# Performance work log

Measured on AMD Instinct MI355X. Metric: run time of the kernel, lower is better.

## Reference

```python
import jax, jax.numpy as jnp
import numpy as np

# 3D multi-scale deformable attention (MSDeformAttn, n_heads=8 / 3D variant)
LEVEL_SHAPES = [(32, 32, 32), (16, 16, 16), (8, 8, 8), (4, 4, 4)]  # (H, W, D) per level
D_MODEL, N_HEADS, N_LEVELS, N_POINTS = 256, 8, 4, 4
C_HEAD = D_MODEL // N_HEADS  # 32
N_BATCH, LEN_Q = 1, 37440
LEN_IN = sum(h * w * d for h, w, d in LEVEL_SHAPES)  # 37440


def setup_inputs() -> dict:
    key = jax.random.key(0)
    ks = jax.random.split(key, 10)
    s = 0.02  # param init scale
    return {
        "query": jax.random.normal(ks[0], (N_BATCH, LEN_Q, D_MODEL), jnp.float32),
        "reference_points": jax.random.uniform(ks[1], (N_BATCH, LEN_Q, N_LEVELS, 3), jnp.float32),
        "input_flatten": jax.random.normal(ks[2], (N_BATCH, LEN_IN, D_MODEL), jnp.float32),
        "input_spatial_shapes": jnp.array(LEVEL_SHAPES, dtype=jnp.int32),
        "input_level_start_index": jnp.array(
            np.cumsum([0] + [h * w * d for h, w, d in LEVEL_SHAPES])[:-1], dtype=jnp.int32),
        "W_value": s * jax.random.normal(ks[3], (D_MODEL, D_MODEL), jnp.float32),
        "b_value": jnp.zeros((D_MODEL,), jnp.float32),
        "W_off": s * jax.random.normal(ks[4], (D_MODEL, N_HEADS * N_LEVELS * N_POINTS * 3), jnp.float32),
        "b_off": s * jax.random.normal(ks[5], (N_HEADS * N_LEVELS * N_POINTS * 3,), jnp.float32),
        "W_attn": s * jax.random.normal(ks[6], (D_MODEL, N_HEADS * N_LEVELS * N_POINTS), jnp.float32),
        "b_attn": jnp.zeros((N_HEADS * N_LEVELS * N_POINTS,), jnp.float32),
        "W_out": s * jax.random.normal(ks[7], (D_MODEL, D_MODEL), jnp.float32),
        "b_out": jnp.zeros((D_MODEL,), jnp.float32),
    }


def trilinear_sample(vol, gx, gy, gz):
    """torch F.grid_sample 3D, mode=bilinear, padding=zeros, align_corners=False.
    vol: (B, C, Dz, Dy, Dx); gx indexes Dx, gy indexes Dy, gz indexes Dz, each (B, Q) in [-1,1].
    Returns (B, C, Q)."""
    B, C, Dz, Dy, Dx = vol.shape
    ix = ((gx + 1.0) * Dx - 1.0) * 0.5
    iy = ((gy + 1.0) * Dy - 1.0) * 0.5
    iz = ((gz + 1.0) * Dz - 1.0) * 0.5
    x0f, y0f, z0f = jnp.floor(ix), jnp.floor(iy), jnp.floor(iz)
    fx, fy, fz = ix - x0f, iy - y0f, iz - z0f
    x0, y0, z0 = x0f.astype(jnp.int32), y0f.astype(jnp.int32), z0f.astype(jnp.int32)
    vol_f = vol.reshape(B, C, Dz * Dy * Dx)
    out = jnp.zeros((B, C, gx.shape[1]), vol.dtype)
    for dz in (0, 1):
        for dy in (0, 1):
            for dx in (0, 1):
                xc, yc, zc = x0 + dx, y0 + dy, z0 + dz
                w = ((fx if dx else 1.0 - fx) * (fy if dy else 1.0 - fy) * (fz if dz else 1.0 - fz))
                valid = ((xc >= 0) & (xc < Dx) & (yc >= 0) & (yc < Dy) & (zc >= 0) & (zc < Dz))
                idx = (jnp.clip(zc, 0, Dz - 1) * Dy + jnp.clip(yc, 0, Dy - 1)) * Dx + jnp.clip(xc, 0, Dx - 1)
                v = jnp.take_along_axis(vol_f, idx[:, None, :], axis=2)  # (B, C, Q)
                out = out + (w * valid.astype(w.dtype))[:, None, :] * v
    return out


def reference(query, reference_points, input_flatten, input_spatial_shapes,
              input_level_start_index, W_value, b_value, W_off, b_off,
              W_attn, b_attn, W_out, b_out):
    N, Lq, _ = query.shape
    Lin = input_flatten.shape[1]
    value = (input_flatten @ W_value + b_value).reshape(N, Lin, N_HEADS, C_HEAD)
    off = (query @ W_off + b_off).reshape(N, Lq, N_HEADS, N_LEVELS, N_POINTS, 3)
    attn = jax.nn.softmax((query @ W_attn + b_attn).reshape(N, Lq, N_HEADS, N_LEVELS * N_POINTS), axis=-1)
    # offset_normalizer = [W, H, D] per level (as in the torch code)
    norm = jnp.stack([input_spatial_shapes[:, 1], input_spatial_shapes[:, 0],
                      input_spatial_shapes[:, 2]], -1).astype(query.dtype)
    loc = reference_points[:, :, None, :, None, :] + off / norm[None, None, None, :, None, :]
    grids = 2.0 * loc - 1.0  # (N, Lq, M, L, P, 3)
    starts = np.cumsum([0] + [h * w * d for h, w, d in LEVEL_SHAPES])
    sampled = []
    for l, (H, W, D) in enumerate(LEVEL_SHAPES):
        vl = value[:, starts[l]:starts[l + 1]]  # (N, H*W*D, M, C)
        vol = (vl.reshape(N, H, W, D, N_HEADS, C_HEAD)
                 .transpose(0, 4, 5, 1, 2, 3)
                 .reshape(N * N_HEADS, C_HEAD, H, W, D))
        g = grids[:, :, :, l].transpose(0, 2, 1, 3, 4).reshape(N * N_HEADS, Lq * N_POINTS, 3)
        # grid x indexes last vol dim (D), y indexes W, z indexes H (torch grid_sample convention)
        s = trilinear_sample(vol, g[..., 0], g[..., 1], g[..., 2])  # (N*M, C, Lq*P)
        sampled.append(s.reshape(N * N_HEADS, C_HEAD, Lq, N_POINTS))
    samp = jnp.stack(sampled, axis=-2).reshape(N * N_HEADS, C_HEAD, Lq, N_LEVELS * N_POINTS)
    aw = attn.transpose(0, 2, 1, 3).reshape(N * N_HEADS, 1, Lq, N_LEVELS * N_POINTS)
    out = (samp * aw).sum(-1).reshape(N, N_HEADS * C_HEAD, Lq).transpose(0, 2, 1)
    return out @ W_out + b_out
```

## Files before the change

### kernel.cpp

```cpp
#include <hip/hip_runtime.h>
#include <math.h>

#define LQ      37440
#define LIN     37440
#define DMODEL  256
#define NHEADS  8
#define CHEAD   32
#define K_DIM   256

#define VALB_DELTA (LIN * 256 + 32)

typedef __attribute__((ext_vector_type(8))) short short8;
typedef __attribute__((ext_vector_type(4))) short short4v;
typedef __attribute__((ext_vector_type(4))) float f32x4;
typedef __attribute__((ext_vector_type(2))) float f32x2;

__device__ inline unsigned short bf16_rte(float f) {
    union { float f; unsigned u; } v; v.f = f;
    return (unsigned short)((v.u + 0x7fffu + ((v.u >> 16) & 1u)) >> 16);
}
__device__ inline float bf16_f(unsigned short s) {
    union { unsigned u; float f; } v; v.u = ((unsigned)s) << 16;
    return v.f;
}
__device__ inline float bits_f(unsigned u) {
    union { unsigned u; float f; } v; v.u = u;
    return v.f;
}
__device__ inline unsigned pkbf(float a, float b) {
    return (unsigned)bf16_rte(a) | ((unsigned)bf16_rte(b) << 16);
}

__device__ __forceinline__ void gl_lds16(const unsigned short* g, unsigned short* l) {
    __builtin_amdgcn_global_load_lds(
        (const __attribute__((address_space(1))) void*)g,
        (__attribute__((address_space(3))) void*)l, 16, 0, 0);
}

__global__ __launch_bounds__(256) void prep_all(
        const float* __restrict__ inp, const float* __restrict__ query,
        const float* __restrict__ Wv, const float* __restrict__ Wo,
        const float* __restrict__ Wa, const float* __restrict__ Wout,
        const float* __restrict__ bo, const float* __restrict__ ba,
        unsigned short* __restrict__ in_b, unsigned short* __restrict__ q_b,
        unsigned short* __restrict__ Bv, unsigned short* __restrict__ Bq,
        unsigned short* __restrict__ Bw, float* __restrict__ bias_m,
        unsigned short* __restrict__ padA,
        unsigned short* __restrict__ valB,
        int n4)
{
    const int bid = blockIdx.x;
    if (bid < 9360) {
        int i = bid * 256 + threadIdx.x;
        int j = i * 2;
        const float* src;
        unsigned short* dst;
        int jj;
        if (j < n4) { src = inp;   dst = in_b; jj = j; }
        else        { src = query; dst = q_b;  jj = j - n4; }
        float4 v0 = ((const float4*)src)[jj];
        float4 v1 = ((const float4*)src)[jj + 1];
        int4 o;
        o.x = (int)pkbf(v0.x, v0.y);
        o.y = (int)pkbf(v0.z, v0.w);
        o.z = (int)pkbf(v1.x, v1.y);
        o.w = (int)pkbf(v1.z, v1.w);
        ((int4*)dst)[jj >> 1] = o;
    } else {
        int i = (bid - 9360) * 256 + threadIdx.x;
        int n = i >> 8, k = i & 255;
        if (n < 256) {
            Bv[(size_t)n * 256 + k] = bf16_rte(Wv[(size_t)k * 256 + n]);
        } else if (n < 640) {
            int m = n - 256;
            Bq[(size_t)m * 256 + k] = bf16_rte(Wo[(size_t)k * 384 + m]);
        } else if (n < 768) {
            int m = n - 640;
            Bq[(size_t)(384 + m) * 256 + k] = bf16_rte(Wa[(size_t)k * 128 + m]);
        } else {
            int m = n - 768;
            Bw[(size_t)m * 256 + k] = bf16_rte(Wout[(size_t)k * 256 + m]);
        }
        if (i < 512) bias_m[i] = (i < 384) ? bo[i] : ba[i - 384];
        if (i < 64)       padA[i] = 0;
        else if (i < 96)  valB[i - 64] = 0;
        else if (i < 192) valB[(size_t)LIN * 256 + 32 + (i - 96)] = 0;
    }
}

__global__ __launch_bounds__(256) void gemm2(
    const unsigned short* __restrict__ in_b, const unsigned short* __restrict__ q_b,
    const unsigned short* __restrict__ Bv,   const unsigned short* __restrict__ Bq,
    const float* __restrict__ bv, const float* __restrict__ bias_m,
    unsigned short* __restrict__ value_t, unsigned short* __restrict__ valB,
    unsigned short* __restrict__ qbuf)
{
    __shared__ __align__(16) unsigned short SH[16384];
    unsigned short* AsL = SH;
    unsigned short* BsL = SH + 8192;

    const int t    = threadIdx.x;
    const int bm   = blockIdx.y * 128;
    const int w    = t >> 6;
    const int lane = t & 63;
    const int lm   = lane & 15;
    const int quad = lane >> 4;

    const int isval = (blockIdx.x < 2);
    const unsigned short* A  = isval ? in_b : q_b;
    const unsigned short* Bt = isval ? Bv : Bq;
    const float* bias        = isval ? bv : bias_m;
    const int n0             = (isval ? blockIdx.x : (blockIdx.x - 2)) * 128;

    const unsigned short* ga[2]; const unsigned short* gb[2];
    int loff[2];
    #pragma unroll
    for (int i = 0; i < 2; ++i) {
        int idx = i * 256 + t;
        int row = idx >> 2;
        int chn = (idx & 3) ^ ((row >> 1) & 3);
        int rga = bm + row; if (rga >= LQ) rga = LQ - 1;
        ga[i] = A  + (size_t)rga * K_DIM + chn * 8;
        gb[i] = Bt + (size_t)(n0 + row) * K_DIM + chn * 8;
        loff[i] = i * 2048 + w * 512;
    }

    const int ra0 = w * 32 + lm, ra1 = ra0 + 16;
    const int aoff0 = ra0 * 32 + ((quad ^ ((ra0 >> 1) & 3)) << 3);
    const int aoff1 = ra1 * 32 + ((quad ^ ((ra1 >> 1) & 3)) << 3);
    int boff[8];
    #pragma unroll
    for (int nt = 0; nt < 8; ++nt) {
        int rb = nt * 16 + lm;
        boff[nt] = rb * 32 + ((quad ^ ((rb >> 1) & 3)) << 3);
    }

    f32x4 acc[2][8];
    #pragma unroll
    for (int mt = 0; mt < 2; ++mt)
        #pragma unroll
        for (int nt = 0; nt < 8; ++nt)
            acc[mt][nt] = (f32x4){0.f, 0.f, 0.f, 0.f};

    #define STAGE(K0, SEL) do { \
        gl_lds16(ga[0] + (K0), AsL + (SEL) * 4096 + loff[0]); \
        gl_lds16(ga[1] + (K0), AsL + (SEL) * 4096 + loff[1]); \
        gl_lds16(gb[0] + (K0), BsL + (SEL) * 4096 + loff[0]); \
        gl_lds16(gb[1] + (K0), BsL + (SEL) * 4096 + loff[1]); \
    } while (0)

    STAGE(0, 0);
    #pragma unroll
    for (int kt = 0; kt < 8; ++kt) {
        const int sel = kt & 1;
        if (kt < 7) {
            STAGE((kt + 1) * 32, sel ^ 1);
            asm volatile("s_waitcnt vmcnt(4)" ::: "memory");
        } else {
            asm volatile("s_waitcnt vmcnt(0)" ::: "memory");
        }
        __builtin_amdgcn_s_barrier();

        const int so = sel * 4096;
        short8 af[2], bf[8];
        af[0] = *(const short8*)&AsL[so + aoff0];
        af[1] = *(const short8*)&AsL[so + aoff1];
        #pragma unroll
        for (int nt = 0; nt < 8; ++nt)
            bf[nt] = *(const short8*)&BsL[so + boff[nt]];
        #pragma unroll
        for (int mt = 0; mt < 2; ++mt)
            #pragma unroll
            for (int nt = 0; nt < 8; ++nt)
                acc[mt][nt] = __builtin_amdgcn_mfma_f32_16x16x32_bf16(af[mt], bf[nt], acc[mt][nt], 0, 0, 0);

        asm volatile("s_waitcnt lgkmcnt(0)" ::: "memory");
        __builtin_amdgcn_s_barrier();
    }
    #undef STAGE

    unsigned short* SHc = SH;
    #pragma unroll
    for (int nt = 0; nt < 8; ++nt) {
        int col = nt * 16 + lm;
        float bb = bias[n0 + col];
        #pragma unroll
        for (int mt = 0; mt < 2; ++mt) {
            int rb = w * 32 + mt * 16 + quad * 4;
            #pragma unroll
            for (int r = 0; r < 4; ++r)
                SHc[(rb + r) * 128 + col] = bf16_rte(acc[mt][nt][r] + bb);
        }
    }
    __syncthreads();

    if (isval) {
        const int h0 = n0 >> 5;
        #pragma unroll
        for (int k = 0; k < 8; ++k) {
            int ci  = t + k * 256;
            int hl  = ci >> 9;
            int rem = ci & 511;
            int row = rem >> 2;
            int cq  = (rem & 3) << 3;
            int4 v = *(const int4*)&SHc[row * 128 + hl * 32 + cq];
            int grow = bm + row;
            if (grow < LQ) {
                size_t e = ((size_t)(h0 + hl) * LIN + grow) * 32 + cq;
                *(int4*)&value_t[e] = v;
                *(int4*)&valB[32 + e] = v;
            }
        }
    } else {
        #pragma unroll
        for (int k = 0; k < 8; ++k) {
            int ci  = t + k * 256;
            int row = ci >> 4;
            int cq  = (ci & 15) << 3;
            int4 v = *(const int4*)&SHc[row * 128 + cq];
            int grow = bm + row;
            if (grow < LQ)
                *(int4*)&qbuf[(size_t)grow * 512 + n0 + cq] = v;
        }
    }
}

__global__ __launch_bounds__(256) void gemm_out(
    const unsigned short* __restrict__ A, const unsigned short* __restrict__ Bt,
    const float* __restrict__ bias, float* __restrict__ Cout)
{
    __shared__ __align__(16) unsigned short SH[16384];
    unsigned short* AsL = SH;
    unsigned short* BsL = SH + 8192;

    const int t    = threadIdx.x;
    const int bm   = blockIdx.y * 128;
    const int n0   = blockIdx.x * 128;
    const int w    = t >> 6;
    const int lane = t & 63;
    const int lm   = lane & 15;
    const int quad = lane >> 4;

    const unsigned short* ga[2]; const unsigned short* gb[2];
    int loff[2];
    #pragma unroll
    for (int i = 0; i < 2; ++i) {
        int idx = i * 256 + t;
        int row = idx >> 2;
        int chn = (idx & 3) ^ ((row >> 1) & 3);
        int rga = bm + row; if (rga >= LQ) rga = LQ - 1;
        ga[i] = A  + (size_t)rga * K_DIM + chn * 8;
        gb[i] = Bt + (size_t)(n0 + row) * K_DIM + chn * 8;
        loff[i] = i * 2048 + w * 512;
    }

    const int ra0 = w * 32 + lm, ra1 = ra0 + 16;
    const int aoff0 = ra0 * 32 + ((quad ^ ((ra0 >> 1) & 3)) << 3);
    const int aoff1 = ra1 * 32 + ((quad ^ ((ra1 >> 1) & 3)) << 3);
    int boff[8];
    #pragma unroll
    for (int nt = 0; nt < 8; ++nt) {
        int rb = nt * 16 + lm;
        boff[nt] = rb * 32 + ((quad ^ ((rb >> 1) & 3)) << 3);
    }

    f32x4 acc[2][8];
    #pragma unroll
    for (int mt = 0; mt < 2; ++mt)
        #pragma unroll
        for (int nt = 0; nt < 8; ++nt)
            acc[mt][nt] = (f32x4){0.f, 0.f, 0.f, 0.f};

    #define STAGE(K0, SEL) do { \
        gl_lds16(ga[0] + (K0), AsL + (SEL) * 4096 + loff[0]); \
        gl_lds16(ga[1] + (K0), AsL + (SEL) * 4096 + loff[1]); \
        gl_lds16(gb[0] + (K0), BsL + (SEL) * 4096 + loff[0]); \
        gl_lds16(gb[1] + (K0), BsL + (SEL) * 4096 + loff[1]); \
    } while (0)

    STAGE(0, 0);
    #pragma unroll
    for (int kt = 0; kt < 8; ++kt) {
        const int sel = kt & 1;
        if (kt < 7) {
            STAGE((kt + 1) * 32, sel ^ 1);
            asm volatile("s_waitcnt vmcnt(4)" ::: "memory");
        } else {
            asm volatile("s_waitcnt vmcnt(0)" ::: "memory");
        }
        __builtin_amdgcn_s_barrier();

        const int so = sel * 4096;
        short8 af[2], bf[8];
        af[0] = *(const short8*)&AsL[so + aoff0];
        af[1] = *(const short8*)&AsL[so + aoff1];
        #pragma unroll
        for (int nt = 0; nt < 8; ++nt)
            bf[nt] = *(const short8*)&BsL[so + boff[nt]];
        #pragma unroll
        for (int mt = 0; mt < 2; ++mt)
            #pragma unroll
            for (int nt = 0; nt < 8; ++nt)
                acc[mt][nt] = __builtin_amdgcn_mfma_f32_16x16x32_bf16(af[mt], bf[nt], acc[mt][nt], 0, 0, 0);

        asm volatile("s_waitcnt lgkmcnt(0)" ::: "memory");
        __builtin_amdgcn_s_barrier();
    }
    #undef STAGE

    float* SHf = (float*)SH;
    #pragma unroll
    for (int p = 0; p < 2; ++p) {
        if (p) __syncthreads();
        #pragma unroll
        for (int nt = 0; nt < 8; ++nt) {
            int col = nt * 16 + lm;
            float bb = bias[n0 + col];
            int lrow = w * 16 + quad * 4;
            #pragma unroll
            for (int r = 0; r < 4; ++r)
                SHf[(lrow + r) * 128 + col] = acc[p][nt][r] + bb;
        }
        __syncthreads();
        #pragma unroll
        for (int k = 0; k < 8; ++k) {
            int ci  = t + k * 256;
            int lr  = ci >> 5;
            int cq  = (ci & 31) << 2;
            int4 v = *(const int4*)&SHf[lr * 128 + cq];
            int grow = bm + (lr >> 4) * 32 + p * 16 + (lr & 15);
            if (grow < LQ)
                *(int4*)&Cout[(size_t)grow * 256 + n0 + cq] = v;
        }
    }
}

__global__ __launch_bounds__(256) void sample_kernel(
    const float* __restrict__ refp,
    const unsigned short* __restrict__ qbuf,
    const unsigned short* __restrict__ value_t,
    unsigned short* __restrict__ samp)
{
    __shared__ float4 zywS[4][16][8];
    __shared__ f32x2  wxS [4][16][8];
    __shared__ int4   ozyS[4][16][8];

    const int t  = threadIdx.x;
    const int q0 = blockIdx.x * 4;

    const int   Sz[4]   = {32, 16, 8, 4};
    const float invS[4] = {1.f/32.f, 1.f/16.f, 1.f/8.f, 1.f/4.f};
    const int   St[4]   = {0, 32768, 36864, 37376};

    #pragma unroll
    for (int pi = t; pi < 512; pi += 256) {
        int ql = pi >> 7;
        int hp = pi & 127;
        int hh = hp >> 4;
        int c  = hp & 15;
        int l  = c >> 2;
        int q  = q0 + ql;
        const unsigned short* o = qbuf + (size_t)q * 512 + hp * 3;
        const float* r = refp + q * 12 + l * 3;
        const int   S  = Sz[l];
        const float Sf = (float)S;
        const float is = invS[l];
        float ix = (r[0] + bf16_f(o[0]) * is) * Sf - 0.5f;
        float iy = (r[1] + bf16_f(o[1]) * is) * Sf - 0.5f;
        float iz = (r[2] + bf16_f(o[2]) * is) * Sf - 0.5f;
        float xf = floorf(ix), yf = floorf(iy), zf = floorf(iz);
        float fx = ix - xf, fy = iy - yf, fz = iz - zf;
        int x0 = (int)xf, y0 = (int)yf, z0 = (int)zf;

        float wx0 = (x0 >= 0  && x0 < S)     ? (1.f - fx) : 0.f;
        float wx1 = (x0 >= -1 && x0 < S - 1) ? fx         : 0.f;
        float wy0 = (y0 >= 0  && y0 < S)     ? (1.f - fy) : 0.f;
        float wy1 = (y0 >= -1 && y0 < S - 1) ? fy         : 0.f;
        float wz0 = (z0 >= 0  && z0 < S)     ? (1.f - fz) : 0.f;
        float wz1 = (z0 >= -1 && z0 < S - 1) ? fz         : 0.f;

        int cy0 = min(max(y0, 0), S - 1), cy1 = min(max(y0 + 1, 0), S - 1);
        int cz0 = min(max(z0, 0), S - 1), cz1 = min(max(z0 + 1, 0), S - 1);

        float lgv = bf16_f(qbuf[(size_t)q * 512 + 384 + hp]);
        float m = fmaxf(lgv, __shfl_xor(lgv, 1));
        m = fmaxf(m, __shfl_xor(m, 2));
        m = fmaxf(m, __shfl_xor(m, 4));
        m = fmaxf(m, __shfl_xor(m, 8));
        float e = __expf(lgv - m);
        float s = e + __shfl_xor(e, 1);
        s += __shfl_xor(s, 2);
        s += __shfl_xor(s, 4);
        s += __shfl_xor(s, 8);
        float a = __fdividef(e, s);

        const int S2 = S * S;
        const int st = St[l];
        const int xb = x0 * 32 + ((x0 & 1) ? VALB_DELTA : 0);
        zywS[ql][c][hh] = make_float4(wz0*wy0, wz0*wy1, wz1*wy0, wz1*wy1);
        wxS [ql][c][hh] = (f32x2){wx0 * a, wx1 * a};
        ozyS[ql][c][hh] = make_int4((st + cz0*S2 + cy0*S) * 32 + xb,
                                    (st + cz0*S2 + cy1*S) * 32 + xb,
                                    (st + cz1*S2 + cy0*S) * 32 + xb,
                                    (st + cz1*S2 + cy1*S) * 32 + xb);
    }
    __syncthreads();

    const int ql   = t >> 6;
    const int lane = t & 63;
    const int hh   = lane >> 3;
    const int j    = lane & 7;
    const int xsel = j >> 2;
    const int cgrp = (j & 3) << 3;
    const int q    = q0 + ql;

    const unsigned short* vbase = value_t - 64;
    const unsigned laneoff = (unsigned)(hh * (LIN * 32) + j * 8 + 64);

    f32x2 acc0 = {0.f,0.f}, acc1 = {0.f,0.f}, acc2 = {0.f,0.f}, acc3 = {0.f,0.f};

    #pragma unroll
    for (int c = 0; c < 16; ++c) {
        float4 zyw = zywS[ql][c][hh];
        f32x2  wx  = wxS [ql][c][hh];
        int4   zo  = ozyS[ql][c][hh];
        float  ws  = xsel ? wx.y : wx.x;

        #define CORNER(OFF, WZ) { \
            int4 v = *(const int4*)(vbase + (laneoff + (unsigned)(OFF))); \
            float w_ = (WZ) * ws; \
            f32x2 w2 = {w_, w_}; \
            acc0 += w2 * (f32x2){bits_f(((unsigned)v.x) << 16), bits_f((unsigned)v.x)}; \
            acc1 += w2 * (f32x2){bits_f(((unsigned)v.y) << 16), bits_f((unsigned)v.y)}; \
            acc2 += w2 * (f32x2){bits_f(((unsigned)v.z) << 16), bits_f((unsigned)v.z)}; \
            acc3 += w2 * (f32x2){bits_f(((unsigned)v.w) << 16), bits_f((unsigned)v.w)}; }

        CORNER(zo.x, zyw.x);
        CORNER(zo.y, zyw.y);
        CORNER(zo.z, zyw.z);
        CORNER(zo.w, zyw.w);
        #undef CORNER
    }

    float c0 = acc0.x + __shfl_xor(acc0.x, 4);
    float c1 = acc0.y + __shfl_xor(acc0.y, 4);
    float c2 = acc1.x + __shfl_xor(acc1.x, 4);
    float c3 = acc1.y + __shfl_xor(acc1.y, 4);
    float c4 = acc2.x + __shfl_xor(acc2.x, 4);
    float c5 = acc2.y + __shfl_xor(acc2.y, 4);
    float c6 = acc3.x + __shfl_xor(acc3.x, 4);
    float c7 = acc3.y + __shfl_xor(acc3.y, 4);
    if (xsel == 0) {
        int4 o = make_int4((int)pkbf(c0, c1), (int)pkbf(c2, c3),
                           (int)pkbf(c4, c5), (int)pkbf(c6, c7));
        *(int4*)(samp + (size_t)q * DMODEL + hh * CHEAD + cgrp) = o;
    }
}

extern "C" void kernel_launch(void* const* d_in, const int* in_sizes, int n_in,
                              void* d_out, int out_size, void* d_ws, size_t ws_size,
                              hipStream_t stream) {
    const float* query = (const float*)d_in[0];
    const float* refp  = (const float*)d_in[1];
    const float* inp   = (const float*)d_in[2];
    const float* Wv   = (const float*)d_in[5];
    const float* bv   = (const float*)d_in[6];
    const float* Wo   = (const float*)d_in[7];
    const float* bo   = (const float*)d_in[8];
    const float* Wa   = (const float*)d_in[9];
    const float* ba   = (const float*)d_in[10];
    const float* Wout = (const float*)d_in[11];
    const float* bout = (const float*)d_in[12];

    char* p = (char*)d_ws;
    p += 256;
    unsigned short* value_t = (unsigned short*)p; p += (size_t)LIN * 256 * 2;
    unsigned short* valB    = (unsigned short*)p; p += ((size_t)LIN * 256 + 128) * 2;
    unsigned short* qbuf    = (unsigned short*)p; p += (size_t)LQ * 512 * 2;
    unsigned short* samp    = (unsigned short*)p; p += (size_t)LQ * 256 * 2;
    unsigned short* in_b    = (unsigned short*)p; p += (size_t)LQ * 256 * 2;
    unsigned short* q_b     = (unsigned short*)p; p += (size_t)LQ * 256 * 2;
    unsigned short* Bv   = (unsigned short*)p;    p += 256 * 256 * 2;
    unsigned short* Bq   = (unsigned short*)p;    p += 512 * 256 * 2;
    unsigned short* Bw   = (unsigned short*)p;    p += 256 * 256 * 2;
    float* bias_m = (float*)p;                    p += 512 * 4;

    const int n4 = LQ * 256 / 4;
    dim3 blk(256);

    prep_all<<<9360 + 1024, blk, 0, stream>>>(
        inp, query, Wv, Wo, Wa, Wout, bo, ba,
        in_b, q_b, Bv, Bq, Bw, bias_m, value_t - 64, valB, n4);
    gemm2<<<dim3(6, (LQ + 127) / 128), blk, 0, stream>>>(
        in_b, q_b, Bv, Bq, bv, bias_m, value_t, valB, qbuf);
    sample_kernel<<<LQ / 4, blk, 0, stream>>>(refp, qbuf, value_t, samp);
    gemm_out<<<dim3(2, (LQ + 127) / 128), blk, 0, stream>>>(samp, Bw, bout, (float*)d_out);
}
```

Baseline: 295.1 us.

## Load GEMM A operand directly to registers, remap blocks per XCD, split sampling launch

Both GEMM kernels now load the A operand straight from global memory into MFMA fragment registers, double-buffered, instead of staging it through LDS. This removes half the LDS traffic and the A-side LDS reads. The block index is also remapped so that consecutive tiles land on the same XCD, aiming for better L2 locality. The sampling kernel is split into two half-size launches selected by a qbase offset, which adds launch overhead without an obvious benefit. Direct global loads of A per k-step may be less coalesced than the old LDS staging path.

```diff
diff --git a/kernel.cpp b/kernel.cpp
--- a/kernel.cpp
+++ b/kernel.cpp
@@ -96,38 +96,43 @@
     unsigned short* __restrict__ qbuf)
 {
     __shared__ __align__(16) unsigned short SH[16384];
-    unsigned short* AsL = SH;
-    unsigned short* BsL = SH + 8192;
+    unsigned short* BsL = SH;
 
     const int t    = threadIdx.x;
-    const int bm   = blockIdx.y * 128;
     const int w    = t >> 6;
     const int lane = t & 63;
     const int lm   = lane & 15;
     const int quad = lane >> 4;
 
-    const int isval = (blockIdx.x < 2);
+    const int g   = blockIdx.y * 6 + blockIdx.x;
+    const int xcd = g & 7, idx = g >> 3;
+    const int wg  = (xcd < 6 ? xcd * 220 : 1320 + (xcd - 6) * 219) + idx;
+    const int bx  = wg % 6;
+    const int by  = wg / 6;
+    const int bm  = by * 128;
+
+    const int isval = (bx < 2);
     const unsigned short* A  = isval ? in_b : q_b;
     const unsigned short* Bt = isval ? Bv : Bq;
     const float* bias        = isval ? bv : bias_m;
-    const int n0             = (isval ? blockIdx.x : (blockIdx.x - 2)) * 128;
-
-    const unsigned short* ga[2]; const unsigned short* gb[2];
-    int loff[2];
+    const int n0             = (isval ? bx : (bx - 2)) * 128;
+
+    const unsigned short* gb[2]; int loffB[2];
     #pragma unroll
     for (int i = 0; i < 2; ++i) {
-        int idx = i * 256 + t;
-        int row = idx >> 2;
-        int chn = (idx & 3) ^ ((row >> 1) & 3);
-        int rga = bm + row; if (rga >= LQ) rga = LQ - 1;
-        ga[i] = A  + (size_t)rga * K_DIM + chn * 8;
+        int idx2 = i * 256 + t;
+        int row = idx2 >> 2;
+        int chn = (idx2 & 3) ^ ((row >> 1) & 3);
         gb[i] = Bt + (size_t)(n0 + row) * K_DIM + chn * 8;
-        loff[i] = i * 2048 + w * 512;
+        loffB[i] = i * 2048 + w * 512;
     }
 
     const int ra0 = w * 32 + lm, ra1 = ra0 + 16;
-    const int aoff0 = ra0 * 32 + ((quad ^ ((ra0 >> 1) & 3)) << 3);
-    const int aoff1 = ra1 * 32 + ((quad ^ ((ra1 >> 1) & 3)) << 3);
+    int r0c = bm + ra0; if (r0c >= LQ) r0c = LQ - 1;
+    int r1c = bm + ra1; if (r1c >= LQ) r1c = LQ - 1;
+    const unsigned short* gA0 = A + (size_t)r0c * K_DIM + quad * 8;
+    const unsigned short* gA1 = A + (size_t)r1c * K_DIM + quad * 8;
+
     int boff[8];
     #pragma unroll
     for (int nt = 0; nt < 8; ++nt) {
@@ -142,19 +147,22 @@
         for (int nt = 0; nt < 8; ++nt)
             acc[mt][nt] = (f32x4){0.f, 0.f, 0.f, 0.f};
 
-    #define STAGE(K0, SEL) do { \
-        gl_lds16(ga[0] + (K0), AsL + (SEL) * 4096 + loff[0]); \
-        gl_lds16(ga[1] + (K0), AsL + (SEL) * 4096 + loff[1]); \
-        gl_lds16(gb[0] + (K0), BsL + (SEL) * 4096 + loff[0]); \
-        gl_lds16(gb[1] + (K0), BsL + (SEL) * 4096 + loff[1]); \
-    } while (0)
-
-    STAGE(0, 0);
+    #define GLB(K0, SEL) do { \
+        gl_lds16(gb[0] + (K0), BsL + (SEL) * 4096 + loffB[0]); \
+        gl_lds16(gb[1] + (K0), BsL + (SEL) * 4096 + loffB[1]); } while (0)
+
+    short8 afb[2][2];
+    afb[0][0] = *(const short8*)gA0;
+    afb[0][1] = *(const short8*)gA1;
+    GLB(0, 0);
+
     #pragma unroll
     for (int kt = 0; kt < 8; ++kt) {
         const int sel = kt & 1;
         if (kt < 7) {
-            STAGE((kt + 1) * 32, sel ^ 1);
+            afb[sel ^ 1][0] = *(const short8*)(gA0 + (kt + 1) * 32);
+            afb[sel ^ 1][1] = *(const short8*)(gA1 + (kt + 1) * 32);
+            GLB((kt + 1) * 32, sel ^ 1);
             asm volatile("s_waitcnt vmcnt(4)" ::: "memory");
         } else {
             asm volatile("s_waitcnt vmcnt(0)" ::: "memory");
@@ -162,9 +170,7 @@
         __builtin_amdgcn_s_barrier();
 
         const int so = sel * 4096;
-        short8 af[2], bf[8];
-        af[0] = *(const short8*)&AsL[so + aoff0];
-        af[1] = *(const short8*)&AsL[so + aoff1];
+        short8 bf[8];
         #pragma unroll
         for (int nt = 0; nt < 8; ++nt)
             bf[nt] = *(const short8*)&BsL[so + boff[nt]];
@@ -172,12 +178,12 @@
         for (int mt = 0; mt < 2; ++mt)
             #pragma unroll
             for (int nt = 0; nt < 8; ++nt)
-                acc[mt][nt] = __builtin_amdgcn_mfma_f32_16x16x32_bf16(af[mt], bf[nt], acc[mt][nt], 0, 0, 0);
+                acc[mt][nt] = __builtin_amdgcn_mfma_f32_16x16x32_bf16(afb[sel][mt], bf[nt], acc[mt][nt], 0, 0, 0);
 
         asm volatile("s_waitcnt lgkmcnt(0)" ::: "memory");
         __builtin_amdgcn_s_barrier();
     }
-    #undef STAGE
+    #undef GLB
 
     unsigned short* SHc = SH;
     #pragma unroll
@@ -230,33 +236,36 @@
     const float* __restrict__ bias, float* __restrict__ Cout)
 {
     __shared__ __align__(16) unsigned short SH[16384];
-    unsigned short* AsL = SH;
-    unsigned short* BsL = SH + 8192;
+    unsigned short* BsL = SH;
 
     const int t    = threadIdx.x;
-    const int bm   = blockIdx.y * 128;
-    const int n0   = blockIdx.x * 128;
     const int w    = t >> 6;
     const int lane = t & 63;
     const int lm   = lane & 15;
     const int quad = lane >> 4;
 
-    const unsigned short* ga[2]; const unsigned short* gb[2];
-    int loff[2];
+    const int g   = blockIdx.y * 2 + blockIdx.x;
+    const int xcd = g & 7, idx = g >> 3;
+    const int wg  = (xcd < 2 ? xcd * 74 : 148 + (xcd - 2) * 73) + idx;
+    const int n0  = (wg % 2) * 128;
+    const int bm  = (wg / 2) * 128;
+
+    const unsigned short* gb[2]; int loffB[2];
     #pragma unroll
     for (int i = 0; i < 2; ++i) {
-        int idx = i * 256 + t;
-        int row = idx >> 2;
-        int chn = (idx & 3) ^ ((row >> 1) & 3);
-        int rga = bm + row; if (rga >= LQ) rga = LQ - 1;
-        ga[i] = A  + (size_t)rga * K_DIM + chn * 8;
+        int idx2 = i * 256 + t;
+        int row = idx2 >> 2;
+        int chn = (idx2 & 3) ^ ((row >> 1) & 3);
         gb[i] = Bt + (size_t)(n0 + row) * K_DIM + chn * 8;
-        loff[i] = i * 2048 + w * 512;
+        loffB[i] = i * 2048 + w * 512;
     }
 
     const int ra0 = w * 32 + lm, ra1 = ra0 + 16;
-    const int aoff0 = ra0 * 32 + ((quad ^ ((ra0 >> 1) & 3)) << 3);
-    const int aoff1 = ra1 * 32 + ((quad ^ ((ra1 >> 1) & 3)) << 3);
+    int r0c = bm + ra0; if (r0c >= LQ) r0c = LQ - 1;
+    int r1c = bm + ra1; if (r1c >= LQ) r1c = LQ - 1;
+    const unsigned short* gA0 = A + (size_t)r0c * K_DIM + quad * 8;
+    const unsigned short* gA1 = A + (size_t)r1c * K_DIM + quad * 8;
+
     int boff[8];
     #pragma unroll
     for (int nt = 0; nt < 8; ++nt) {
@@ -271,19 +280,22 @@
         for (int nt = 0; nt < 8; ++nt)
             acc[mt][nt] = (f32x4){0.f, 0.f, 0.f, 0.f};
 
-    #define STAGE(K0, SEL) do { \
-        gl_lds16(ga[0] + (K0), AsL + (SEL) * 4096 + loff[0]); \
-        gl_lds16(ga[1] + (K0), AsL + (SEL) * 4096 + loff[1]); \
-        gl_lds16(gb[0] + (K0), BsL + (SEL) * 4096 + loff[0]); \
-        gl_lds16(gb[1] + (K0), BsL + (SEL) * 4096 + loff[1]); \
-    } while (0)
-
-    STAGE(0, 0);
+    #define GLB(K0, SEL) do { \
+        gl_lds16(gb[0] + (K0), BsL + (SEL) * 4096 + loffB[0]); \
+        gl_lds16(gb[1] + (K0), BsL + (SEL) * 4096 + loffB[1]); } while (0)
+
+    short8 afb[2][2];
+    afb[0][0] = *(const short8*)gA0;
+    afb[0][1] = *(const short8*)gA1;
+    GLB(0, 0);
+
     #pragma unroll
     for (int kt = 0; kt < 8; ++kt) {
         const int sel = kt & 1;
         if (kt < 7) {
-            STAGE((kt + 1) * 32, sel ^ 1);
+            afb[sel ^ 1][0] = *(const short8*)(gA0 + (kt + 1) * 32);
+            afb[sel ^ 1][1] = *(const short8*)(gA1 + (kt + 1) * 32);
+            GLB((kt + 1) * 32, sel ^ 1);
             asm volatile("s_waitcnt vmcnt(4)" ::: "memory");
         } else {
             asm volatile("s_waitcnt vmcnt(0)" ::: "memory");
@@ -291,9 +303,7 @@
         __builtin_amdgcn_s_barrier();
 
         const int so = sel * 4096;
-        short8 af[2], bf[8];
-        af[0] = *(const short8*)&AsL[so + aoff0];
-        af[1] = *(const short8*)&AsL[so + aoff1];
+        short8 bf[8];
         #pragma unroll
         for (int nt = 0; nt < 8; ++nt)
             bf[nt] = *(const short8*)&BsL[so + boff[nt]];
@@ -301,12 +311,12 @@
         for (int mt = 0; mt < 2; ++mt)
             #pragma unroll
             for (int nt = 0; nt < 8; ++nt)
-                acc[mt][nt] = __builtin_amdgcn_mfma_f32_16x16x32_bf16(af[mt], bf[nt], acc[mt][nt], 0, 0, 0);
+                acc[mt][nt] = __builtin_amdgcn_mfma_f32_16x16x32_bf16(afb[sel][mt], bf[nt], acc[mt][nt], 0, 0, 0);
 
         asm volatile("s_waitcnt lgkmcnt(0)" ::: "memory");
         __builtin_amdgcn_s_barrier();
     }
-    #undef STAGE
+    #undef GLB
 
     float* SHf = (float*)SH;
     #pragma unroll
@@ -339,14 +349,15 @@
     const float* __restrict__ refp,
     const unsigned short* __restrict__ qbuf,
     const unsigned short* __restrict__ value_t,
-    unsigned short* __restrict__ samp)
+    unsigned short* __restrict__ samp,
+    int qbase)
 {
     __shared__ float4 zywS[4][16][8];
     __shared__ f32x2  wxS [4][16][8];
     __shared__ int4   ozyS[4][16][8];
 
     const int t  = threadIdx.x;
-    const int q0 = blockIdx.x * 4;
+    const int q0 = qbase + blockIdx.x * 4;
 
     const int   Sz[4]   = {32, 16, 8, 4};
     const float invS[4] = {1.f/32.f, 1.f/16.f, 1.f/8.f, 1.f/4.f};
@@ -493,6 +504,7 @@
         in_b, q_b, Bv, Bq, Bw, bias_m, value_t - 64, valB, n4);
     gemm2<<<dim3(6, (LQ + 127) / 128), blk, 0, stream>>>(
         in_b, q_b, Bv, Bq, bv, bias_m, value_t, valB, qbuf);
-    sample_kernel<<<LQ / 4, blk, 0, stream>>>(refp, qbuf, value_t, samp);
+    sample_kernel<<<LQ / 8, blk, 0, stream>>>(refp, qbuf, value_t, samp, 0);
+    sample_kernel<<<LQ / 8, blk, 0, stream>>>(refp, qbuf, value_t, samp, LQ / 2);
     gemm_out<<<dim3(2, (LQ + 127) / 128), blk, 0, stream>>>(samp, Bw, bout, (float*)d_out);
 }
```

Measured after the change: 306.2 us. +3.8%, slower.
